# Kernel optimization log

Measured on AMD Instinct MI355X. Metric: run time of the kernel, lower is better.

The kernel has to match this reference:

```python
import jax, jax.numpy as jnp
import numpy as np

VOCAB = 50000
D = 256        # embedding_dim = nb_head * size_per_head
H = 8          # nb_head
DH = 32        # size_per_head
B = 8192
L = 64


def setup_inputs() -> dict:
    key = jax.random.key(0)
    ks = jax.random.split(key, 8)
    tokens = jax.random.randint(ks[0], (B, L), 0, VOCAB)
    scale = 0.02
    emb_table = jax.random.normal(ks[1], (VOCAB, D), dtype=jnp.float32) * scale
    WQ = jax.random.normal(ks[2], (D, D), dtype=jnp.float32) * scale
    WK = jax.random.normal(ks[3], (D, D), dtype=jnp.float32) * scale
    WV = jax.random.normal(ks[4], (D, D), dtype=jnp.float32) * scale
    WO = jax.random.normal(ks[5], (D, D), dtype=jnp.float32) * scale
    dense_w = jax.random.normal(ks[6], (D, 1), dtype=jnp.float32) * scale
    dense_b = jnp.zeros((1,), dtype=jnp.float32)
    return {"tokens": tokens, "emb_table": emb_table, "WQ": WQ, "WK": WK,
            "WV": WV, "WO": WO, "dense_w": dense_w, "dense_b": dense_b}


def _fastformer(x, WQ, WK, WV, WO):
    # x: [B, L, D]
    b, l, _ = x.shape
    Q = (x @ WQ).reshape(b, l, H, DH)
    K = (x @ WK).reshape(b, l, H, DH)
    V = (x @ WV).reshape(b, l, H, DH)
    global_q = jnp.mean(Q, axis=1, keepdims=True)   # [B,1,H,DH]
    global_k = jnp.mean(K, axis=1, keepdims=True)
    w = jnp.sum(global_q * K + global_k * Q, axis=-1)  # [B,L,H]
    w = jax.nn.softmax(w, axis=1)                       # softmax over seq
    context = (w[..., None] * V).reshape(b, l, D)
    return context @ WO


def reference(tokens, emb_table, WQ, WK, WV, WO, dense_w, dense_b):
    # NewsEncoder forward (inference: dropout = identity; masks computed but
    # unused by Fastformer.call, matching the original code).
    title_emb = emb_table[tokens]                       # [B,L,D]
    hidden = _fastformer(title_emb, WQ, WK, WV, WO)     # [B,L,D]
    scores = (hidden @ dense_w + dense_b)[..., 0]       # [B,L]
    attn = jax.nn.softmax(scores, axis=1)               # over seq
    news_vector = jnp.sum(hidden * attn[..., None], axis=1)  # [B,D]
    return news_vector
```

## Files before the change

### kernel.cpp

```cpp
#include <hip/hip_runtime.h>
#include <cstdint>


using f32x4  = __attribute__((ext_vector_type(4))) float;
using bf16x8 = __attribute__((ext_vector_type(8))) short;

__device__ __forceinline__ unsigned int pack2bf(float a, float b) {
  unsigned int ua = __builtin_bit_cast(unsigned int, a);
  unsigned int ub = __builtin_bit_cast(unsigned int, b);
  ua = (ua + 0x7fffu + ((ua >> 16) & 1u)) >> 16;
  ub = (ub + 0x7fffu + ((ub >> 16) & 1u)) >> 16;
  return ua | (ub << 16);
}
__device__ __forceinline__ unsigned short bf1(float a) {
  unsigned int ua = __builtin_bit_cast(unsigned int, a);
  ua = (ua + 0x7fffu + ((ua >> 16) & 1u)) >> 16;
  return (unsigned short)ua;
}
__device__ __forceinline__ float ubf(unsigned int u) {
  return __builtin_bit_cast(float, u << 16);
}

__global__ __launch_bounds__(256) void prep_kernel(const float* __restrict__ WV,
                                                   const float* __restrict__ WO,
                                                   const float* __restrict__ dw,
                                                   unsigned short* __restrict__ mbf) {
  __shared__ float wod[256];
  const int t = threadIdx.x;
  float acc = 0.f;
  for (int e = 0; e < 256; e += 4) {
    const float4 w4 = *(const float4*)(WO + (size_t)t * 256 + e);
    const float4 d4 = *(const float4*)(dw + e);
    acc += w4.x * d4.x + w4.y * d4.y + w4.z * d4.z + w4.w * d4.w;
  }
  wod[t] = acc;
  __syncthreads();
  for (int h = 0; h < 8; ++h) {
    float a = 0.f;
    for (int j = 0; j < 32; j += 4) {
      const float4 w4 = *(const float4*)(WV + (size_t)t * 256 + h * 32 + j);
      a += w4.x * wod[h*32+j] + w4.y * wod[h*32+j+1] + w4.z * wod[h*32+j+2] + w4.w * wod[h*32+j+3];
    }
    const float o = __shfl_xor(a, 1);
    if (!(t & 1)) ((unsigned int*)mbf)[h * 128 + (t >> 1)] = pack2bf(a, o);
  }
}

__global__ __launch_bounds__(256) void prep_T(const float* __restrict__ WQ,
                                              const float* __restrict__ WK,
                                              unsigned short* __restrict__ tkn) {
  __shared__ float ek[8][32], eq[8][32];
  const int t = threadIdx.x;
  const int n0 = blockIdx.x * 8;
  const int h  = n0 >> 8;
  {
    const int ei = t >> 5, j = t & 31;
    const int e = (n0 & 255) + ei;
    ek[ei][j] = WK[(size_t)e * 256 + h * 32 + j];
    eq[ei][j] = WQ[(size_t)e * 256 + h * 32 + j];
  }
  __syncthreads();
  float wqd[32], wkd[32];
#pragma unroll
  for (int j = 0; j < 32; j += 4) {
    *(float4*)(wqd + j) = *(const float4*)(WQ + (size_t)t * 256 + h * 32 + j);
    *(float4*)(wkd + j) = *(const float4*)(WK + (size_t)t * 256 + h * 32 + j);
  }
#pragma unroll
  for (int ei = 0; ei < 8; ++ei) {
    float a = 0.f;
#pragma unroll
    for (int j = 0; j < 32; ++j) a += wqd[j] * ek[ei][j] + wkd[j] * eq[ei][j];
    const float o = __shfl_xor(a, 1);
    if (!(t & 1)) ((unsigned int*)tkn)[(size_t)(n0 + ei) * 128 + (t >> 1)] = pack2bf(a, o);
  }
}

__global__ __launch_bounds__(256) void prep_P(const float* __restrict__ WV,
                                              const float* __restrict__ WO,
                                              unsigned short* __restrict__ ptb) {
  __shared__ float wvs[32][32];
  __shared__ float wos[32][256];
  const int t = threadIdx.x;
  const int h = blockIdx.x, d0 = blockIdx.y * 32;
  {
    const int dd = t >> 3, jq = (t & 7) * 4;
    *(float4*)(&wvs[dd][jq]) = *(const float4*)(WV + (size_t)(d0 + dd) * 256 + h * 32 + jq);
    const int c4 = (t & 63) * 4;
#pragma unroll
    for (int jj = 0; jj < 8; ++jj) {
      const int j = (t >> 6) * 8 + jj;
      *(float4*)(&wos[j][c4]) = *(const float4*)(WO + (size_t)(h * 32 + j) * 256 + c4);
    }
  }
  __syncthreads();
  const int n = t;
#pragma unroll 4
  for (int dd = 0; dd < 32; ++dd) {
    float a = 0.f;
#pragma unroll
    for (int j = 0; j < 32; ++j) a += wvs[dd][j] * wos[j][n];
    ptb[(size_t)n * 2048 + h * 256 + d0 + dd] = bf1(a);
  }
}

__global__ __launch_bounds__(256) void ebf_kernel(const float4* __restrict__ emb4,
                                                  uint2* __restrict__ out2, int n) {
  for (int i = blockIdx.x * 256 + threadIdx.x; i < n; i += gridDim.x * 256) {
    const float4 v = emb4[i];
    uint2 pk;
    pk.x = pack2bf(v.x, v.y);
    pk.y = pack2bf(v.z, v.w);
    out2[i] = pk;
  }
}

__global__ __launch_bounds__(256) void xbar_kernel(const int* __restrict__ tokens,
                                                   const unsigned short* __restrict__ ebf,
                                                   unsigned short* __restrict__ xbf) {
  __shared__ int tok[64];
  __shared__ float part[4][64][4];
  const int b = blockIdx.x, t = threadIdx.x;
  if (t < 64) tok[t] = tokens[b * 64 + t];
  __syncthreads();
  const int cp = t & 63, rg = t >> 6;
  const uint2* e2 = (const uint2*)ebf;
  float s0 = 0.f, s1 = 0.f, s2 = 0.f, s3 = 0.f;
#pragma unroll
  for (int ri = 0; ri < 16; ++ri) {
    const uint2 u = e2[(size_t)tok[rg * 16 + ri] * 64 + cp];
    s0 += ubf(u.x & 0xffffu); s1 += ubf(u.x >> 16);
    s2 += ubf(u.y & 0xffffu); s3 += ubf(u.y >> 16);
  }
  *(float4*)part[rg][cp] = make_float4(s0, s1, s2, s3);
  __syncthreads();
  if (t < 64) {
    const float4 p0 = *(const float4*)part[0][t];
    const float4 p1 = *(const float4*)part[1][t];
    const float4 p2 = *(const float4*)part[2][t];
    const float4 p3 = *(const float4*)part[3][t];
    const float a0 = (p0.x + p1.x + p2.x + p3.x) * (1.f / 64.f);
    const float a1 = (p0.y + p1.y + p2.y + p3.y) * (1.f / 64.f);
    const float a2 = (p0.z + p1.z + p2.z + p3.z) * (1.f / 64.f);
    const float a3 = (p0.w + p1.w + p2.w + p3.w) * (1.f / 64.f);
    uint2 pk;
    pk.x = pack2bf(a0, a1);
    pk.y = pack2bf(a2, a3);
    *(uint2*)((unsigned int*)xbf + (size_t)b * 128 + 2 * t) = pk;
  }
}

__global__ __launch_bounds__(256) void cgemm(const unsigned short* __restrict__ xbf,
                                             const unsigned short* __restrict__ tkn,
                                             unsigned short* __restrict__ cbf) {
  __shared__ unsigned short As[64 * 264];
  const int t = threadIdx.x;
  const int m0 = blockIdx.x * 64, n0 = blockIdx.y * 64;
#pragma unroll
  for (int it = 0; it < 8; ++it) {
    const int idx = it * 256 + t;
    const int row = idx >> 5, c = idx & 31;
    const uint4 v = *(const uint4*)(xbf + (size_t)(m0 + row) * 256 + c * 8);
    *(uint4*)(As + row * 264 + c * 8) = v;
  }
  __syncthreads();
  const int wv = t >> 6, l = t & 63;
  const int g = l >> 4, r = l & 15;
#pragma unroll
  for (int nt = 0; nt < 4; ++nt) {
    const int n = n0 + nt * 16 + r;
    f32x4 acc = {0.f, 0.f, 0.f, 0.f};
#pragma unroll
    for (int kk = 0; kk < 8; ++kk) {
      const bf16x8 a  = *(const bf16x8*)(As + (16 * wv + r) * 264 + kk * 32 + g * 8);
      const bf16x8 bb = *(const bf16x8*)(tkn + (size_t)n * 256 + kk * 32 + g * 8);
      acc = __builtin_amdgcn_mfma_f32_16x16x32_bf16(a, bb, acc, 0, 0, 0);
    }
#pragma unroll
    for (int i = 0; i < 4; ++i)
      cbf[(size_t)(m0 + 16 * wv + g * 4 + i) * 2048 + n] = bf1(acc[i]);
  }
}

__global__ __launch_bounds__(256) void main_kernel(const int* __restrict__ tokens,
                                                   const unsigned short* __restrict__ ebf,
                                                   const unsigned short* __restrict__ mbf,
                                                   const float* __restrict__ dense_b,
                                                   unsigned short* __restrict__ cbf) {
  __shared__ unsigned short xl[64 * 264];
  __shared__ float wslds[64 * 17];
  __shared__ unsigned short cfT[16 * 80];
  const int t = threadIdx.x;
  const int b = blockIdx.x;
  const int wv = t >> 6, l = t & 63;
  const int g = l >> 4, r = l & 15;
  {
    unsigned int* cz = (unsigned int*)(cfT + 8 * 80);
    for (int z = t; z < 320; z += 256) cz[z] = 0u;
  }
  {
    const uint4* eb4 = (const uint4*)ebf;
#pragma unroll
    for (int it = 0; it < 8; ++it) {
      const int idx = it * 256 + t;
      const int row = idx >> 5, c = idx & 31;
      const int tk = tokens[b * 64 + row];
      *(uint4*)(xl + row * 264 + c * 8) = eb4[(size_t)tk * 32 + c];
    }
  }
  __syncthreads();
  {
    const unsigned short* arow = xl + (16 * wv + r) * 264;
    const unsigned short* brow = (r < 8) ? (cbf + (size_t)b * 2048 + r * 256)
                                         : (mbf + (size_t)(r - 8) * 256);
    f32x4 acc = {0.f, 0.f, 0.f, 0.f};
#pragma unroll
    for (int kk = 0; kk < 8; ++kk) {
      const bf16x8 a  = *(const bf16x8*)(arow + kk * 32 + g * 8);
      const bf16x8 bb = *(const bf16x8*)(brow + kk * 32 + g * 8);
      acc = __builtin_amdgcn_mfma_f32_16x16x32_bf16(a, bb, acc, 0, 0, 0);
    }
#pragma unroll
    for (int i = 0; i < 4; ++i)
      wslds[(16 * wv + g * 4 + i) * 17 + r] = acc[i];
  }
  __syncthreads();
  {
#pragma unroll
    for (int hh = 0; hh < 2; ++hh) {
      const int h = 2 * wv + hh;
      const float v = wslds[l * 17 + h];
      float mx = v;
#pragma unroll
      for (int sft = 32; sft; sft >>= 1) mx = fmaxf(mx, __shfl_xor(mx, sft));
      const float e = expf(v - mx);
      float sm = e;
#pragma unroll
      for (int sft = 32; sft; sft >>= 1) sm += __shfl_xor(sm, sft);
      wslds[l * 17 + h] = e / sm;
    }
  }
  __syncthreads();
  {
    float p[8], sv[8];
#pragma unroll
    for (int h = 0; h < 8; ++h) { p[h] = wslds[l*17 + h]; sv[h] = wslds[l*17 + 8 + h]; }
    float sc = dense_b[0];
#pragma unroll
    for (int h = 0; h < 8; ++h) sc += p[h] * sv[h];
    float mx = sc;
#pragma unroll
    for (int sft = 32; sft; sft >>= 1) mx = fmaxf(mx, __shfl_xor(mx, sft));
    const float e = expf(sc - mx);
    float sm = e;
#pragma unroll
    for (int sft = 32; sft; sft >>= 1) sm += __shfl_xor(sm, sft);
    const float attn = e / sm;
    float cc0, cc1;
    if      (wv == 0) { cc0 = attn * p[0]; cc1 = attn * p[1]; }
    else if (wv == 1) { cc0 = attn * p[2]; cc1 = attn * p[3]; }
    else if (wv == 2) { cc0 = attn * p[4]; cc1 = attn * p[5]; }
    else              { cc0 = attn * p[6]; cc1 = attn * p[7]; }
    cfT[(2 * wv) * 80 + l]     = bf1(cc0);
    cfT[(2 * wv + 1) * 80 + l] = bf1(cc1);
  }
  __syncthreads();
  {
    const bf16x8 a0 = *(const bf16x8*)(cfT + r * 80 + g * 8);
    const bf16x8 a1 = *(const bf16x8*)(cfT + r * 80 + 32 + g * 8);
    const short* xs = (const short*)xl;
#pragma unroll
    for (int nt = 0; nt < 4; ++nt) {
      const int d = wv * 64 + nt * 16 + r;
      short bv0[8], bv1[8];
#pragma unroll
      for (int j = 0; j < 8; ++j) {
        bv0[j] = xs[(g * 8 + j) * 264 + d];
        bv1[j] = xs[(32 + g * 8 + j) * 264 + d];
      }
      f32x4 acc = {0.f, 0.f, 0.f, 0.f};
      acc = __builtin_amdgcn_mfma_f32_16x16x32_bf16(a0, *(const bf16x8*)bv0, acc, 0, 0, 0);
      acc = __builtin_amdgcn_mfma_f32_16x16x32_bf16(a1, *(const bf16x8*)bv1, acc, 0, 0, 0);
      if (g < 2) {
#pragma unroll
        for (int i = 0; i < 4; ++i) {
          const int h = g * 4 + i;
          cbf[(size_t)b * 2048 + h * 256 + d] = bf1(acc[i]);
        }
      }
    }
  }
}

__global__ __launch_bounds__(256) void pgemm(const unsigned short* __restrict__ cbf,
                                             const unsigned short* __restrict__ ptb,
                                             float* __restrict__ out) {
  __shared__ unsigned short As[64 * 264];
  const int t = threadIdx.x;
  const int m0 = blockIdx.x * 64, n0 = blockIdx.y * 64;
  const int wv = t >> 6, l = t & 63;
  const int g = l >> 4, r = l & 15;
  f32x4 acc[4] = {};
  for (int kc = 0; kc < 8; ++kc) {
    __syncthreads();
#pragma unroll
    for (int it = 0; it < 8; ++it) {
      const int idx = it * 256 + t;
      const int row = idx >> 5, c = idx & 31;
      const uint4 v = *(const uint4*)(cbf + (size_t)(m0 + row) * 2048 + kc * 256 + c * 8);
      *(uint4*)(As + row * 264 + c * 8) = v;
    }
    __syncthreads();
#pragma unroll
    for (int kk = 0; kk < 8; ++kk) {
      const bf16x8 a = *(const bf16x8*)(As + (16 * wv + r) * 264 + kk * 32 + g * 8);
#pragma unroll
      for (int nt = 0; nt < 4; ++nt) {
        const int n = n0 + nt * 16 + r;
        const bf16x8 bb = *(const bf16x8*)(ptb + (size_t)n * 2048 + kc * 256 + kk * 32 + g * 8);
        acc[nt] = __builtin_amdgcn_mfma_f32_16x16x32_bf16(a, bb, acc[nt], 0, 0, 0);
      }
    }
  }
#pragma unroll
  for (int nt = 0; nt < 4; ++nt) {
    const int n = n0 + nt * 16 + r;
#pragma unroll
    for (int i = 0; i < 4; ++i)
      out[(size_t)(m0 + 16 * wv + g * 4 + i) * 256 + n] = acc[nt][i];
  }
}

extern "C" void kernel_launch(void* const* d_in, const int* in_sizes, int n_in,
                              void* d_out, int out_size, void* d_ws, size_t ws_size,
                              hipStream_t stream) {
  const int*   tokens = (const int*)d_in[0];
  const float* emb    = (const float*)d_in[1];
  const float* WQ     = (const float*)d_in[2];
  const float* WK     = (const float*)d_in[3];
  const float* WV     = (const float*)d_in[4];
  const float* WO     = (const float*)d_in[5];
  const float* dw     = (const float*)d_in[6];
  const float* db     = (const float*)d_in[7];
  float* out = (float*)d_out;

  unsigned short* base = (unsigned short*)d_ws;
  unsigned short* mbf  = base;
  unsigned short* xbf  = base + 2048;
  unsigned short* tkn  = xbf + (size_t)8192 * 256;
  unsigned short* cbf  = tkn + (size_t)2048 * 256;
  unsigned short* ebf  = cbf + (size_t)8192 * 2048;
  unsigned short* ptb  = ebf + (size_t)50000 * 256;

  const size_t need_bytes = (size_t)(2048 + 8192*256 + 2048*256 + 8192*2048
                                     + 50000*256 + 256*2048) * 2;
  if (ws_size < need_bytes) return;

  prep_kernel<<<dim3(1), dim3(256), 0, stream>>>(WV, WO, dw, mbf);
  prep_T<<<dim3(256), dim3(256), 0, stream>>>(WQ, WK, tkn);
  prep_P<<<dim3(8, 8), dim3(256), 0, stream>>>(WV, WO, ptb);
  ebf_kernel<<<dim3(2048), dim3(256), 0, stream>>>((const float4*)emb, (uint2*)ebf,
                                                   50000 * 64);
  xbar_kernel<<<dim3(8192), dim3(256), 0, stream>>>(tokens, ebf, xbf);
  cgemm<<<dim3(128, 32), dim3(256), 0, stream>>>(xbf, tkn, cbf);
  main_kernel<<<dim3(8192), dim3(256), 0, stream>>>(tokens, ebf, mbf, db, cbf);
  pgemm<<<dim3(128, 4), dim3(256), 0, stream>>>(cbf, ptb, out);
}
```

Before: 274.6 us.

## Use direct global-to-LDS loads with XOR swizzle; halve pgemm M tile

The embedding gather in main_kernel now uses global_load_lds to write 16-byte chunks straight into shared memory. Padding is dropped in favour of an XOR swizzle, and both MFMA read paths are updated to match. Separately, pgemm uses 32-row M tiles with waves split over M and N halves, doubling the grid size. The intent is to skip the register round-trip on the gather and to raise pgemm parallelism, at the cost of more redundant B loads in pgemm.

```diff
diff --git a/kernel.cpp b/kernel.cpp
--- a/kernel.cpp
+++ b/kernel.cpp
@@ -19,6 +19,11 @@
 }
 __device__ __forceinline__ float ubf(unsigned int u) {
   return __builtin_bit_cast(float, u << 16);
+}
+__device__ __forceinline__ void gload_lds16(const void* g, void* l) {
+  __builtin_amdgcn_global_load_lds(
+      (const __attribute__((address_space(1))) void*)g,
+      (__attribute__((address_space(3))) void*)l, 16, 0, 0);
 }
 
 __global__ __launch_bounds__(256) void prep_kernel(const float* __restrict__ WV,
@@ -187,7 +192,7 @@
                                                    const unsigned short* __restrict__ mbf,
                                                    const float* __restrict__ dense_b,
                                                    unsigned short* __restrict__ cbf) {
-  __shared__ unsigned short xl[64 * 264];
+  __shared__ unsigned short xl[64 * 256];
   __shared__ float wslds[64 * 17];
   __shared__ unsigned short cfT[16 * 80];
   const int t = threadIdx.x;
@@ -199,24 +204,27 @@
     for (int z = t; z < 320; z += 256) cz[z] = 0u;
   }
   {
-    const uint4* eb4 = (const uint4*)ebf;
+    const int ln = t & 63;
 #pragma unroll
     for (int it = 0; it < 8; ++it) {
-      const int idx = it * 256 + t;
-      const int row = idx >> 5, c = idx & 31;
-      const int tk = tokens[b * 64 + row];
-      *(uint4*)(xl + row * 264 + c * 8) = eb4[(size_t)tk * 32 + c];
-    }
-  }
-  __syncthreads();
-  {
-    const unsigned short* arow = xl + (16 * wv + r) * 264;
+      const int R0 = it * 8 + wv * 2;
+      const int R  = R0 + (ln >> 5);
+      const int j  = ln & 31;
+      const int tk = tokens[b * 64 + R];
+      const unsigned short* src = ebf + (size_t)tk * 256 + ((j ^ (R & 7)) << 3);
+      gload_lds16(src, (void*)(xl + R0 * 256));
+    }
+  }
+  __syncthreads();
+  {
+    const unsigned short* arow = xl + (16 * wv + r) * 256;
+    const int sw = r & 7;
     const unsigned short* brow = (r < 8) ? (cbf + (size_t)b * 2048 + r * 256)
                                          : (mbf + (size_t)(r - 8) * 256);
     f32x4 acc = {0.f, 0.f, 0.f, 0.f};
 #pragma unroll
     for (int kk = 0; kk < 8; ++kk) {
-      const bf16x8 a  = *(const bf16x8*)(arow + kk * 32 + g * 8);
+      const bf16x8 a  = *(const bf16x8*)(arow + (((kk * 4 + g) ^ sw) << 3));
       const bf16x8 bb = *(const bf16x8*)(brow + kk * 32 + g * 8);
       acc = __builtin_amdgcn_mfma_f32_16x16x32_bf16(a, bb, acc, 0, 0, 0);
     }
@@ -275,8 +283,9 @@
       short bv0[8], bv1[8];
 #pragma unroll
       for (int j = 0; j < 8; ++j) {
-        bv0[j] = xs[(g * 8 + j) * 264 + d];
-        bv1[j] = xs[(32 + g * 8 + j) * 264 + d];
+        const int off = ((((d >> 3) ^ j) << 3) | (d & 7));
+        bv0[j] = xs[(g * 8 + j) * 256 + off];
+        bv1[j] = xs[(32 + g * 8 + j) * 256 + off];
       }
       f32x4 acc = {0.f, 0.f, 0.f, 0.f};
       acc = __builtin_amdgcn_mfma_f32_16x16x32_bf16(a0, *(const bf16x8*)bv0, acc, 0, 0, 0);
@@ -295,16 +304,17 @@
 __global__ __launch_bounds__(256) void pgemm(const unsigned short* __restrict__ cbf,
                                              const unsigned short* __restrict__ ptb,
                                              float* __restrict__ out) {
-  __shared__ unsigned short As[64 * 264];
-  const int t = threadIdx.x;
-  const int m0 = blockIdx.x * 64, n0 = blockIdx.y * 64;
+  __shared__ unsigned short As[32 * 264];
+  const int t = threadIdx.x;
+  const int m0 = blockIdx.x * 32, n0 = blockIdx.y * 64;
   const int wv = t >> 6, l = t & 63;
   const int g = l >> 4, r = l & 15;
-  f32x4 acc[4] = {};
+  const int msub = wv & 1, nhalf = wv >> 1;
+  f32x4 acc[2] = {};
   for (int kc = 0; kc < 8; ++kc) {
     __syncthreads();
 #pragma unroll
-    for (int it = 0; it < 8; ++it) {
+    for (int it = 0; it < 4; ++it) {
       const int idx = it * 256 + t;
       const int row = idx >> 5, c = idx & 31;
       const uint4 v = *(const uint4*)(cbf + (size_t)(m0 + row) * 2048 + kc * 256 + c * 8);
@@ -313,21 +323,21 @@
     __syncthreads();
 #pragma unroll
     for (int kk = 0; kk < 8; ++kk) {
-      const bf16x8 a = *(const bf16x8*)(As + (16 * wv + r) * 264 + kk * 32 + g * 8);
-#pragma unroll
-      for (int nt = 0; nt < 4; ++nt) {
-        const int n = n0 + nt * 16 + r;
+      const bf16x8 a = *(const bf16x8*)(As + (16 * msub + r) * 264 + kk * 32 + g * 8);
+#pragma unroll
+      for (int nt = 0; nt < 2; ++nt) {
+        const int n = n0 + (nhalf * 2 + nt) * 16 + r;
         const bf16x8 bb = *(const bf16x8*)(ptb + (size_t)n * 2048 + kc * 256 + kk * 32 + g * 8);
         acc[nt] = __builtin_amdgcn_mfma_f32_16x16x32_bf16(a, bb, acc[nt], 0, 0, 0);
       }
     }
   }
 #pragma unroll
-  for (int nt = 0; nt < 4; ++nt) {
-    const int n = n0 + nt * 16 + r;
+  for (int nt = 0; nt < 2; ++nt) {
+    const int n = n0 + (nhalf * 2 + nt) * 16 + r;
 #pragma unroll
     for (int i = 0; i < 4; ++i)
-      out[(size_t)(m0 + 16 * wv + g * 4 + i) * 256 + n] = acc[nt][i];
+      out[(size_t)(m0 + 16 * msub + g * 4 + i) * 256 + n] = acc[nt][i];
   }
 }
 
@@ -364,5 +374,5 @@
   xbar_kernel<<<dim3(8192), dim3(256), 0, stream>>>(tokens, ebf, xbf);
   cgemm<<<dim3(128, 32), dim3(256), 0, stream>>>(xbf, tkn, cbf);
   main_kernel<<<dim3(8192), dim3(256), 0, stream>>>(tokens, ebf, mbf, db, cbf);
-  pgemm<<<dim3(128, 4), dim3(256), 0, stream>>>(cbf, ptb, out);
-}
+  pgemm<<<dim3(256, 4), dim3(256), 0, stream>>>(cbf, ptb, out);
+}
```

Measured after the change: 275.1 us. Within noise of the previous version (+0.2%).
